# Optimization experiments

Measured on AMD Instinct MI355X. Metric: run time of the kernel, lower is better.

Reference implementation:

```python
import jax, jax.numpy as jnp
import numpy as np

N, C, H, W = 8, 256, 128, 128
K = 7            # cls_p
HID = 10         # hidden_dim
OUT_C = (K - 1) * HID  # 60
BN_EPS = 1e-5


def setup_inputs() -> dict:
    key = jax.random.key(0)
    ks = jax.random.split(key, 7)
    return {
        "p_fea": jax.random.normal(ks[0], (N, C, H, W), jnp.float32),
        "p_seg": jax.random.normal(ks[1], (N, K, H, W), jnp.float32),
        "Wq": jax.random.normal(ks[2], (HID, C), jnp.float32) * 0.05,
        "bq": jax.random.normal(ks[3], (HID,), jnp.float32) * 0.05,
        "Wk": jax.random.normal(ks[4], (HID, C), jnp.float32) * 0.05,
        "bk": jax.random.normal(ks[5], (HID,), jnp.float32) * 0.05,
        "Wp": jax.random.normal(ks[6], (OUT_C, 2 * C), jnp.float32) * 0.05,
        "gamma": jnp.ones((OUT_C,), jnp.float32),
        "beta": jnp.zeros((OUT_C,), jnp.float32),
    }


def reference(p_fea, p_seg, Wq, bq, Wk, bk, Wp, gamma, beta):
    n, c, h, w = p_fea.shape
    hw = h * w
    fea = p_fea.reshape(n, c, hw)                      # [n,c,s]
    # class-center pooling: softmax over class dim, weighted mean of features
    att = jax.nn.softmax(p_seg.reshape(n, K, hw), axis=1)      # [n,k,s]
    num = jnp.einsum('ncs,nks->nck', fea, att)                 # [n,c,k]
    den = jnp.sum(att, axis=2)[:, None, :]                     # [n,1,k]
    p_center = num / den                                        # [n,c,k]
    # 1x1 conv1d / conv2d == matmul over channel dim
    query = jnp.einsum('oc,nck->nok', Wq, p_center) + bq[None, :, None]  # [n,hid,k]
    key_ = jnp.einsum('oc,ncs->nos', Wk, fea) + bk[None, :, None]        # [n,hid,s]
    energy = jnp.einsum('nok,nos->nks', query, key_)                     # [n,k,s]
    attention = jax.nn.softmax(energy, axis=1)                           # over class dim
    new_fea = jnp.einsum('nck,nks->ncs', p_center, attention).reshape(n, c, h, w)
    # project: concat -> 1x1 conv (no bias) -> BN (batch stats) -> ReLU
    x = jnp.concatenate([p_fea, new_fea], axis=1)              # [n,2c,h,w]
    y = jnp.einsum('oc,nchw->nohw', Wp, x)                     # [n,60,h,w]
    mean = jnp.mean(y, axis=(0, 2, 3))
    var = jnp.var(y, axis=(0, 2, 3))
    y = (y - mean[None, :, None, None]) * jax.lax.rsqrt(var + BN_EPS)[None, :, None, None]
    y = y * gamma[None, :, None, None] + beta[None, :, None, None]
    y = jnp.maximum(y, 0.0)
    # torch.split(..., HID, dim=1) -> list of (cls_p-1) chunks; return as one axis
    return y.reshape(n, K - 1, HID, h, w)
```

## Files before the change

### kernel.cpp

```cpp
#include <hip/hip_runtime.h>
#include <hip/hip_bf16.h>

#define N_    8
#define C_    256
#define K_    7
#define HID_  10
#define OUTC_ 60
#define S_    16384
#define BN_EPS 1e-5f

#define OFF_PP     0
#define OFF_DP     1048576
#define OFF_EB     1052672
#define OFF_WB16   1052736
#define OFF_M2B    1151040
#define OFF_PART   1153600
#define OFF_SCL    1276480
#define OFF_SHF    1276544

#define GLDS(g, l) __builtin_amdgcn_global_load_lds( \
    (const __attribute__((address_space(1))) unsigned int*)(g), \
    (__attribute__((address_space(3))) unsigned int*)(l), 16, 0, 0)

typedef __attribute__((ext_vector_type(8))) short bfrag;
typedef __attribute__((ext_vector_type(4))) float f32x4;

static __device__ __forceinline__ unsigned short f2bf(float f) {
    __hip_bfloat16 h = __float2bfloat16(f);
    return *reinterpret_cast<unsigned short*>(&h);
}

__global__ void __launch_bounds__(256) k_pool(
        const float* __restrict__ fea, const float* __restrict__ seg,
        float* __restrict__ pp, float* __restrict__ dp) {
    int g = blockIdx.x;
    int lin = (g & 7) * 64 + (g >> 3);
    int n = lin >> 6, sl = lin & 63;
    int tid = threadIdx.x, lane = tid & 63, wv = tid >> 6;
    int r15 = lane & 15, kg = (lane >> 4) << 3, pg = (lane >> 4) << 2;
    int px0 = sl * 256;

    __shared__ unsigned short attT[16 * 256];
    __shared__ unsigned short feaB[2][256 * 32];
    __shared__ float red[4][8];

    {
        const float* sp = seg + (size_t)n * K_ * S_ + px0 + tid;
        float e[K_], mx = -1e30f;
#pragma unroll
        for (int k = 0; k < K_; k++) { e[k] = sp[(size_t)k * S_]; mx = fmaxf(mx, e[k]); }
        float sum = 0.f;
#pragma unroll
        for (int k = 0; k < K_; k++) { e[k] = __expf(e[k] - mx); sum += e[k]; }
        float inv = 1.f / sum;
#pragma unroll
        for (int k = 0; k < K_; k++) {
            e[k] *= inv;
            attT[k * 256 + tid] = f2bf(e[k]);
        }
#pragma unroll
        for (int k = 0; k < K_; k++) {
            float v = e[k];
            for (int off = 32; off; off >>= 1) v += __shfl_xor(v, off, 64);
            if (lane == 0) red[wv][k] = v;
        }
    }

    const float* fb = fea + (size_t)n * C_ * S_ + px0;
    int pq4 = (tid & 7) * 4;
    int crow = tid >> 3;

    {
        float4 s[8];
#pragma unroll
        for (int rr = 0; rr < 8; rr++)
            s[rr] = *(const float4*)(fb + (size_t)(rr * 32 + crow) * S_ + pq4);
#pragma unroll
        for (int rr = 0; rr < 8; rr++) {
            unsigned int u0 = (unsigned int)f2bf(s[rr].x) | ((unsigned int)f2bf(s[rr].y) << 16);
            unsigned int u1 = (unsigned int)f2bf(s[rr].z) | ((unsigned int)f2bf(s[rr].w) << 16);
            *(uint2*)&feaB[0][(rr * 32 + crow) * 32 + pq4] = make_uint2(u0, u1);
        }
    }
    __syncthreads();
    if (tid < K_)
        dp[(size_t)lin * 8 + tid] = red[0][tid] + red[1][tid] + red[2][tid] + red[3][tid];

    f32x4 acc[4];
#pragma unroll
    for (int mt = 0; mt < 4; mt++) acc[mt] = (f32x4)0.f;

#pragma unroll
    for (int ch = 0; ch < 8; ch++) {
        int cur = ch & 1;
        float4 s[8];
        if (ch < 7) {
#pragma unroll
            for (int rr = 0; rr < 8; rr++)
                s[rr] = *(const float4*)(fb + (size_t)(rr * 32 + crow) * S_ + (ch + 1) * 32 + pq4);
        }
        bfrag b = *(const bfrag*)&attT[r15 * 256 + ch * 32 + kg];
#pragma unroll
        for (int mt = 0; mt < 4; mt++) {
            bfrag a = *(const bfrag*)&feaB[cur][(wv * 64 + mt * 16 + r15) * 32 + kg];
            acc[mt] = __builtin_amdgcn_mfma_f32_16x16x32_bf16(a, b, acc[mt], 0, 0, 0);
        }
        if (ch < 7) {
#pragma unroll
            for (int rr = 0; rr < 8; rr++) {
                unsigned int u0 = (unsigned int)f2bf(s[rr].x) | ((unsigned int)f2bf(s[rr].y) << 16);
                unsigned int u1 = (unsigned int)f2bf(s[rr].z) | ((unsigned int)f2bf(s[rr].w) << 16);
                *(uint2*)&feaB[cur ^ 1][(rr * 32 + crow) * 32 + pq4] = make_uint2(u0, u1);
            }
        }
        __syncthreads();
    }

    if (r15 < K_) {
#pragma unroll
        for (int mt = 0; mt < 4; mt++) {
#pragma unroll
            for (int r = 0; r < 4; r++) {
                int c = wv * 64 + mt * 16 + pg + r;
                pp[((size_t)lin * 256 + c) * 8 + r15] = acc[mt][r];
            }
        }
    }
}

__global__ void k_center(const float* __restrict__ pp, const float* __restrict__ dp,
                         const float* __restrict__ Wq, const float* __restrict__ bq,
                         const float* __restrict__ Wk, const float* __restrict__ bk,
                         const float* __restrict__ Wp,
                         float* __restrict__ eb, float* __restrict__ m2b,
                         float* __restrict__ wb16) {
    int n = blockIdx.x >> 3, j = blockIdx.x & 7;
    int tid = threadIdx.x;
    __shared__ float pc[C_ * K_];
    __shared__ float ql[HID_ * K_];
    __shared__ float dinv[K_];
    if (tid < K_) {
        float d = 0.f;
        for (int s = 0; s < 64; s++) d += dp[(size_t)(n * 64 + s) * 8 + tid];
        dinv[tid] = 1.f / d;
    }
    __syncthreads();
    for (int i = tid; i < C_ * K_; i += 256) {
        int c = i / K_, k = i - c * K_;
        float v = 0.f;
        for (int s = 0; s < 64; s++)
            v += pp[((size_t)(n * 64 + s) * 256 + c) * 8 + k];
        pc[i] = v * dinv[k];
    }
    __syncthreads();
    if (tid < HID_ * K_) {
        int o = tid / K_, k = tid % K_;
        float s = bq[o];
        for (int c = 0; c < C_; c++) s += Wq[o * C_ + c] * pc[c * K_ + k];
        ql[tid] = s;
    }
    __syncthreads();
    unsigned short* wp16 = (unsigned short*)wb16 + (size_t)n * 24576;
    for (int i = j * 3072 + tid; i < (j + 1) * 3072; i += 256) {
        int ch = i / 6144, r = i - ch * 6144;
        int o = r / 72, jj = r - o * 72;
        float v = 0.f;
        if (o < 80 && jj < 64) {
            int c = ch * 64 + jj;
            if (o < 60) v = Wp[o * 2 * C_ + c];
            else if (o < 67) {
                int k = o - 60;
                for (int o2 = 0; o2 < HID_; o2++) v += ql[o2 * K_ + k] * Wk[o2 * C_ + c];
            }
        }
        wp16[i] = f2bf(v);
    }
    unsigned short* mp16 = (unsigned short*)m2b + (size_t)n * 640;
    if (tid < 80) {
        int i = j * 80 + tid;
        int o = i >> 3, k = i & 7;
        float v = 0.f;
        if (k < 7 && o < 60) {
            for (int c = 0; c < C_; c++) v += Wp[o * 2 * C_ + C_ + c] * pc[c * K_ + k];
        }
        mp16[i] = f2bf(v);
    }
    if (j == 0 && tid < K_) {
        float s = 0.f;
        for (int o = 0; o < HID_; o++) s += ql[o * K_ + tid] * bk[o];
        eb[n * K_ + tid] = s;
    }
}

__global__ void __launch_bounds__(256) k_main(
        const float* __restrict__ fea, const float* __restrict__ wb16,
        const float* __restrict__ ebias, const float* __restrict__ m2b,
        float* __restrict__ y, float* __restrict__ part) {
    int g = blockIdx.x;
    int lin = (g & 7) * 128 + (g >> 3);
    int n = lin >> 7, tile = lin & 127;
    int tid = threadIdx.x, lane = tid & 63, wv = tid >> 6;
    int r15 = lane & 15, kg = (lane >> 4) << 3, pg = (lane >> 4) << 2;

    __shared__ unsigned short wlds[2][6144];
    __shared__ unsigned short feaT[2][9216];
    __shared__ unsigned short abf[128 * 8];
    __shared__ unsigned short m2l[640];
    __shared__ float att_e[K_][128];
    __shared__ float ebl[8];
    __shared__ float redm[4][80];
    __shared__ float redq[4][80];

    const unsigned int* wsrc = (const unsigned int*)wb16 + (size_t)n * 12288;
    const unsigned int* m2s  = (const unsigned int*)m2b + (size_t)n * 320;
    for (int i = tid; i < 320; i += 256) ((unsigned int*)m2l)[i] = m2s[i];
    if (tid < K_) ebl[tid] = ebias[n * K_ + tid];

    const float* fbase = fea + (size_t)n * C_ * S_ + tile * 128;
    int cr2 = tid >> 3, h = tid & 7;

    f32x4 acc[5][2];
#pragma unroll
    for (int ot = 0; ot < 5; ot++) { acc[ot][0] = (f32x4)0.f; acc[ot][1] = (f32x4)0.f; }

#pragma unroll
    for (int rnd = 0; rnd < 3; rnd++)
        GLDS(wsrc + rnd * 1024 + wv * 256 + lane * 4,
             &((unsigned int*)wlds[0])[rnd * 1024 + wv * 256]);
    {
        const float* bp = fbase + (size_t)(cr2 * 2) * S_ + h * 16;
        float4 v0[4], v1[4];
#pragma unroll
        for (int i = 0; i < 4; i++) v0[i] = *(const float4*)(bp + i * 4);
#pragma unroll
        for (int i = 0; i < 4; i++) v1[i] = *(const float4*)(bp + S_ + i * 4);
        unsigned int* dst = (unsigned int*)feaT[0];
#pragma unroll
        for (int i = 0; i < 4; i++)
#pragma unroll
            for (int e = 0; e < 4; e++) {
                int px = h * 16 + i * 4 + e;
                dst[px * 36 + cr2] = (unsigned int)f2bf(((const float*)&v0[i])[e])
                                   | ((unsigned int)f2bf(((const float*)&v1[i])[e]) << 16);
            }
    }
    asm volatile("s_waitcnt vmcnt(0) lgkmcnt(0)" ::: "memory");
    __builtin_amdgcn_s_barrier();

#pragma unroll
    for (int ch = 0; ch < 4; ch++) {
        int bb = ch & 1;
        float4 s0[4], s1[4];
        if (ch < 3) {
#pragma unroll
            for (int rnd = 0; rnd < 3; rnd++)
                GLDS(wsrc + (ch + 1) * 3072 + rnd * 1024 + wv * 256 + lane * 4,
                     &((unsigned int*)wlds[bb ^ 1])[rnd * 1024 + wv * 256]);
            const float* bp = fbase + (size_t)((ch + 1) * 64 + cr2 * 2) * S_ + h * 16;
#pragma unroll
            for (int i = 0; i < 4; i++) s0[i] = *(const float4*)(bp + i * 4);
#pragma unroll
            for (int i = 0; i < 4; i++) s1[i] = *(const float4*)(bp + S_ + i * 4);
        }
        const unsigned short* fb = feaT[bb];
        const unsigned short* wb = wlds[bb];
#pragma unroll
        for (int ks = 0; ks < 2; ks++) {
            bfrag a0 = *(const bfrag*)&fb[(wv * 32 + r15) * 72 + ks * 32 + kg];
            bfrag a1 = *(const bfrag*)&fb[(wv * 32 + 16 + r15) * 72 + ks * 32 + kg];
#pragma unroll
            for (int ot = 0; ot < 5; ot++) {
                bfrag b = *(const bfrag*)&wb[(ot * 16 + r15) * 72 + ks * 32 + kg];
                acc[ot][0] = __builtin_amdgcn_mfma_f32_16x16x32_bf16(a0, b, acc[ot][0], 0, 0, 0);
                acc[ot][1] = __builtin_amdgcn_mfma_f32_16x16x32_bf16(a1, b, acc[ot][1], 0, 0, 0);
            }
        }
        if (ch < 3) {
            unsigned int* dst = (unsigned int*)feaT[bb ^ 1];
#pragma unroll
            for (int i = 0; i < 4; i++)
#pragma unroll
                for (int e = 0; e < 4; e++) {
                    int px = h * 16 + i * 4 + e;
                    dst[px * 36 + cr2] = (unsigned int)f2bf(((const float*)&s0[i])[e])
                                       | ((unsigned int)f2bf(((const float*)&s1[i])[e]) << 16);
                }
        }
        asm volatile("s_waitcnt vmcnt(0) lgkmcnt(0)" ::: "memory");
        __builtin_amdgcn_s_barrier();
    }

    if (r15 >= 12) {
        int k = r15 - 12;
#pragma unroll
        for (int pxt = 0; pxt < 2; pxt++)
#pragma unroll
            for (int r = 0; r < 4; r++)
                att_e[k][wv * 32 + pxt * 16 + pg + r] = acc[3][pxt][r];
    }
    if (r15 < 3) {
        int k = 4 + r15;
#pragma unroll
        for (int pxt = 0; pxt < 2; pxt++)
#pragma unroll
            for (int r = 0; r < 4; r++)
                att_e[k][wv * 32 + pxt * 16 + pg + r] = acc[4][pxt][r];
    }
    __syncthreads();
    if (tid < 128) {
        float e[K_], mx = -1e30f;
#pragma unroll
        for (int k = 0; k < K_; k++) { e[k] = att_e[k][tid] + ebl[k]; mx = fmaxf(mx, e[k]); }
        float sum = 0.f;
#pragma unroll
        for (int k = 0; k < K_; k++) { e[k] = __expf(e[k] - mx); sum += e[k]; }
        float inv = 1.f / sum;
        unsigned int* ab = (unsigned int*)abf;
        ab[tid * 4 + 0] = (unsigned int)f2bf(e[0] * inv) | ((unsigned int)f2bf(e[1] * inv) << 16);
        ab[tid * 4 + 1] = (unsigned int)f2bf(e[2] * inv) | ((unsigned int)f2bf(e[3] * inv) << 16);
        ab[tid * 4 + 2] = (unsigned int)f2bf(e[4] * inv) | ((unsigned int)f2bf(e[5] * inv) << 16);
        ab[tid * 4 + 3] = (unsigned int)f2bf(e[6] * inv);
    }
    __syncthreads();

    bfrag az = (bfrag)(short)0;
    bfrag a20 = az, a21 = az;
    if (lane < 16) {
        a20 = *(const bfrag*)&abf[(wv * 32 + r15) * 8];
        a21 = *(const bfrag*)&abf[(wv * 32 + 16 + r15) * 8];
    }
#pragma unroll
    for (int ot = 0; ot < 5; ot++) {
        bfrag b2 = az;
        if (lane < 16) b2 = *(const bfrag*)&m2l[(ot * 16 + r15) * 8];
        acc[ot][0] = __builtin_amdgcn_mfma_f32_16x16x32_bf16(a20, b2, acc[ot][0], 0, 0, 0);
        acc[ot][1] = __builtin_amdgcn_mfma_f32_16x16x32_bf16(a21, b2, acc[ot][1], 0, 0, 0);
    }

    float* ybase = y + (size_t)n * OUTC_ * S_ + tile * 128 + wv * 32 + pg;
#pragma unroll
    for (int ot = 0; ot < 5; ot++) {
        int o = ot * 16 + r15;
        float sm_ = 0.f, sq_ = 0.f;
#pragma unroll
        for (int pxt = 0; pxt < 2; pxt++) {
            f32x4 v = acc[ot][pxt];
            if (o < OUTC_)
                *(f32x4*)(ybase + (size_t)o * S_ + pxt * 16) = v;
            sm_ += v[0] + v[1] + v[2] + v[3];
            sq_ += v[0]*v[0] + v[1]*v[1] + v[2]*v[2] + v[3]*v[3];
        }
        sm_ += __shfl_xor(sm_, 16, 64); sm_ += __shfl_xor(sm_, 32, 64);
        sq_ += __shfl_xor(sq_, 16, 64); sq_ += __shfl_xor(sq_, 32, 64);
        if (lane < 16) { redm[wv][ot * 16 + lane] = sm_; redq[wv][ot * 16 + lane] = sq_; }
    }
    __syncthreads();
    if (tid < 120) {
        float s;
        if (tid < OUTC_)
            s = redm[0][tid] + redm[1][tid] + redm[2][tid] + redm[3][tid];
        else {
            int o = tid - OUTC_;
            s = redq[0][o] + redq[1][o] + redq[2][o] + redq[3][o];
        }
        part[(size_t)g * 120 + tid] = s;
    }
}

__global__ void k_bn(const float* __restrict__ part, const float* __restrict__ gamma,
                     const float* __restrict__ beta, float* __restrict__ scl,
                     float* __restrict__ shf) {
    int t = threadIdx.x & 127, q = threadIdx.x >> 7;
    __shared__ float red[4][120];
    __shared__ float tot[120];
    if (t < 120) {
        float s = 0.f;
        for (int b = q * 256; b < q * 256 + 256; b++) s += part[(size_t)b * 120 + t];
        red[q][t] = s;
    }
    __syncthreads();
    if (threadIdx.x < 120)
        tot[threadIdx.x] = red[0][threadIdx.x] + red[1][threadIdx.x] +
                           red[2][threadIdx.x] + red[3][threadIdx.x];
    __syncthreads();
    if (threadIdx.x < OUTC_) {
        const float invn = 1.f / (float)(N_ * S_);
        float mean = tot[threadIdx.x] * invn;
        float var = tot[60 + threadIdx.x] * invn - mean * mean;
        float sc = gamma[threadIdx.x] * rsqrtf(var + BN_EPS);
        scl[threadIdx.x] = sc;
        shf[threadIdx.x] = beta[threadIdx.x] - mean * sc;
    }
}

__global__ void k_apply(float* __restrict__ y, const float* __restrict__ scl,
                        const float* __restrict__ shf) {
    int idx = blockIdx.x * 256 + threadIdx.x;
    int o = (idx >> 12) % OUTC_;
    float4 v = ((const float4*)y)[idx];
    float a = scl[o], b = shf[o];
    v.x = fmaxf(v.x * a + b, 0.f);
    v.y = fmaxf(v.y * a + b, 0.f);
    v.z = fmaxf(v.z * a + b, 0.f);
    v.w = fmaxf(v.w * a + b, 0.f);
    ((float4*)y)[idx] = v;
}

extern "C" void kernel_launch(void* const* d_in, const int* in_sizes, int n_in,
                              void* d_out, int out_size, void* d_ws, size_t ws_size,
                              hipStream_t stream) {
    const float* p_fea = (const float*)d_in[0];
    const float* p_seg = (const float*)d_in[1];
    const float* Wq    = (const float*)d_in[2];
    const float* bq    = (const float*)d_in[3];
    const float* Wk    = (const float*)d_in[4];
    const float* bk    = (const float*)d_in[5];
    const float* Wp    = (const float*)d_in[6];
    const float* gamma = (const float*)d_in[7];
    const float* beta  = (const float*)d_in[8];

    float* ws   = (float*)d_ws;
    float* pp   = ws + OFF_PP;
    float* dp   = ws + OFF_DP;
    float* eb   = ws + OFF_EB;
    float* wb16 = ws + OFF_WB16;
    float* m2b  = ws + OFF_M2B;
    float* part = ws + OFF_PART;
    float* scl  = ws + OFF_SCL;
    float* shf  = ws + OFF_SHF;
    float* ybuf = (float*)d_out;

    k_pool<<<512, 256, 0, stream>>>(p_fea, p_seg, pp, dp);
    k_center<<<64, 256, 0, stream>>>(pp, dp, Wq, bq, Wk, bk, Wp, eb, m2b, wb16);
    k_main<<<1024, 256, 0, stream>>>(p_fea, wb16, eb, m2b, ybuf, part);
    k_bn<<<1, 512, 0, stream>>>(part, gamma, beta, scl, shf);
    k_apply<<<(N_ * OUTC_ * S_ / 4) / 256, 256, 0, stream>>>(ybuf, scl, shf);
}
```

Baseline: 117.7 us.

## Split pooling channels across blocks and load main-kernel weights into registers

The pooling kernel now splits the 256 channels into two halves per pixel slice, doubling the grid to 1024 blocks and halving its shared memory and accumulators. This should give better occupancy and load balance. The main kernel drops the async global-to-LDS weight staging and instead loads per-chunk weight fragments straight from global memory into registers. Its shared memory is merged into one aliased buffer to shrink the LDS footprint, which needs an extra barrier before the softmax results overwrite the aliased region. The trade-offs are recomputing the softmax over the segmentation map twice per slice and relying on cache hits for the repeated weight loads.

```diff
diff --git a/kernel.cpp b/kernel.cpp
--- a/kernel.cpp
+++ b/kernel.cpp
@@ -18,10 +18,6 @@
 #define OFF_SCL    1276480
 #define OFF_SHF    1276544
 
-#define GLDS(g, l) __builtin_amdgcn_global_load_lds( \
-    (const __attribute__((address_space(1))) unsigned int*)(g), \
-    (__attribute__((address_space(3))) unsigned int*)(l), 16, 0, 0)
-
 typedef __attribute__((ext_vector_type(8))) short bfrag;
 typedef __attribute__((ext_vector_type(4))) float f32x4;
 
@@ -34,14 +30,16 @@
         const float* __restrict__ fea, const float* __restrict__ seg,
         float* __restrict__ pp, float* __restrict__ dp) {
     int g = blockIdx.x;
-    int lin = (g & 7) * 64 + (g >> 3);
-    int n = lin >> 6, sl = lin & 63;
+    int lin = (g & 7) * 128 + (g >> 3);
+    int n = lin >> 7, r = lin & 127;
+    int sl = r >> 1, h2 = r & 1;
+    int c0 = h2 * 128;
+    int px0 = sl * 256;
     int tid = threadIdx.x, lane = tid & 63, wv = tid >> 6;
     int r15 = lane & 15, kg = (lane >> 4) << 3, pg = (lane >> 4) << 2;
-    int px0 = sl * 256;
 
     __shared__ unsigned short attT[16 * 256];
-    __shared__ unsigned short feaB[2][256 * 32];
+    __shared__ unsigned short feaB[2][128 * 32];
     __shared__ float red[4][8];
 
     {
@@ -66,48 +64,48 @@
         }
     }
 
-    const float* fb = fea + (size_t)n * C_ * S_ + px0;
+    const float* fb = fea + ((size_t)n * C_ + c0) * S_ + px0;
     int pq4 = (tid & 7) * 4;
     int crow = tid >> 3;
 
     {
-        float4 s[8];
-#pragma unroll
-        for (int rr = 0; rr < 8; rr++)
+        float4 s[4];
+#pragma unroll
+        for (int rr = 0; rr < 4; rr++)
             s[rr] = *(const float4*)(fb + (size_t)(rr * 32 + crow) * S_ + pq4);
 #pragma unroll
-        for (int rr = 0; rr < 8; rr++) {
+        for (int rr = 0; rr < 4; rr++) {
             unsigned int u0 = (unsigned int)f2bf(s[rr].x) | ((unsigned int)f2bf(s[rr].y) << 16);
             unsigned int u1 = (unsigned int)f2bf(s[rr].z) | ((unsigned int)f2bf(s[rr].w) << 16);
             *(uint2*)&feaB[0][(rr * 32 + crow) * 32 + pq4] = make_uint2(u0, u1);
         }
     }
     __syncthreads();
-    if (tid < K_)
-        dp[(size_t)lin * 8 + tid] = red[0][tid] + red[1][tid] + red[2][tid] + red[3][tid];
-
-    f32x4 acc[4];
-#pragma unroll
-    for (int mt = 0; mt < 4; mt++) acc[mt] = (f32x4)0.f;
+    if (h2 == 0 && tid < K_)
+        dp[(size_t)(n * 64 + sl) * 8 + tid] =
+            red[0][tid] + red[1][tid] + red[2][tid] + red[3][tid];
+
+    f32x4 acc[2];
+    acc[0] = (f32x4)0.f; acc[1] = (f32x4)0.f;
 
 #pragma unroll
     for (int ch = 0; ch < 8; ch++) {
         int cur = ch & 1;
-        float4 s[8];
+        float4 s[4];
         if (ch < 7) {
 #pragma unroll
-            for (int rr = 0; rr < 8; rr++)
+            for (int rr = 0; rr < 4; rr++)
                 s[rr] = *(const float4*)(fb + (size_t)(rr * 32 + crow) * S_ + (ch + 1) * 32 + pq4);
         }
         bfrag b = *(const bfrag*)&attT[r15 * 256 + ch * 32 + kg];
 #pragma unroll
-        for (int mt = 0; mt < 4; mt++) {
-            bfrag a = *(const bfrag*)&feaB[cur][(wv * 64 + mt * 16 + r15) * 32 + kg];
+        for (int mt = 0; mt < 2; mt++) {
+            bfrag a = *(const bfrag*)&feaB[cur][(wv * 32 + mt * 16 + r15) * 32 + kg];
             acc[mt] = __builtin_amdgcn_mfma_f32_16x16x32_bf16(a, b, acc[mt], 0, 0, 0);
         }
         if (ch < 7) {
 #pragma unroll
-            for (int rr = 0; rr < 8; rr++) {
+            for (int rr = 0; rr < 4; rr++) {
                 unsigned int u0 = (unsigned int)f2bf(s[rr].x) | ((unsigned int)f2bf(s[rr].y) << 16);
                 unsigned int u1 = (unsigned int)f2bf(s[rr].z) | ((unsigned int)f2bf(s[rr].w) << 16);
                 *(uint2*)&feaB[cur ^ 1][(rr * 32 + crow) * 32 + pq4] = make_uint2(u0, u1);
@@ -116,13 +114,13 @@
         __syncthreads();
     }
 
-    if (r15 < K_) {
-#pragma unroll
-        for (int mt = 0; mt < 4; mt++) {
-#pragma unroll
-            for (int r = 0; r < 4; r++) {
-                int c = wv * 64 + mt * 16 + pg + r;
-                pp[((size_t)lin * 256 + c) * 8 + r15] = acc[mt][r];
+    if (r15 < 8) {
+#pragma unroll
+        for (int mt = 0; mt < 2; mt++) {
+#pragma unroll
+            for (int rr = 0; rr < 4; rr++) {
+                int c = c0 + wv * 32 + mt * 16 + pg + rr;
+                pp[((size_t)(n * 64 + sl) * 256 + c) * 8 + r15] = acc[mt][rr];
             }
         }
     }
@@ -202,17 +200,18 @@
     int tid = threadIdx.x, lane = tid & 63, wv = tid >> 6;
     int r15 = lane & 15, kg = (lane >> 4) << 3, pg = (lane >> 4) << 2;
 
-    __shared__ unsigned short wlds[2][6144];
-    __shared__ unsigned short feaT[2][9216];
-    __shared__ unsigned short abf[128 * 8];
-    __shared__ unsigned short m2l[640];
-    __shared__ float att_e[K_][128];
-    __shared__ float ebl[8];
-    __shared__ float redm[4][80];
-    __shared__ float redq[4][80];
-
-    const unsigned int* wsrc = (const unsigned int*)wb16 + (size_t)n * 12288;
-    const unsigned int* m2s  = (const unsigned int*)m2b + (size_t)n * 320;
+    __shared__ __align__(16) unsigned char smem[38176];
+    unsigned short* feaT0 = (unsigned short*)smem;
+    unsigned short* feaT1 = (unsigned short*)(smem + 18432);
+    unsigned short* m2l   = (unsigned short*)(smem + 36864);
+    float* ebl            = (float*)(smem + 38144);
+    float* att_e          = (float*)smem;
+    unsigned short* abf   = (unsigned short*)(smem + 3584);
+    float* redm           = (float*)(smem + 5632);
+    float* redq           = (float*)(smem + 6912);
+
+    const unsigned short* wimg = (const unsigned short*)wb16 + (size_t)n * 24576;
+    const unsigned int* m2s = (const unsigned int*)m2b + (size_t)n * 320;
     for (int i = tid; i < 320; i += 256) ((unsigned int*)m2l)[i] = m2s[i];
     if (tid < K_) ebl[tid] = ebias[n * K_ + tid];
 
@@ -223,10 +222,6 @@
 #pragma unroll
     for (int ot = 0; ot < 5; ot++) { acc[ot][0] = (f32x4)0.f; acc[ot][1] = (f32x4)0.f; }
 
-#pragma unroll
-    for (int rnd = 0; rnd < 3; rnd++)
-        GLDS(wsrc + rnd * 1024 + wv * 256 + lane * 4,
-             &((unsigned int*)wlds[0])[rnd * 1024 + wv * 256]);
     {
         const float* bp = fbase + (size_t)(cr2 * 2) * S_ + h * 16;
         float4 v0[4], v1[4];
@@ -234,7 +229,7 @@
         for (int i = 0; i < 4; i++) v0[i] = *(const float4*)(bp + i * 4);
 #pragma unroll
         for (int i = 0; i < 4; i++) v1[i] = *(const float4*)(bp + S_ + i * 4);
-        unsigned int* dst = (unsigned int*)feaT[0];
+        unsigned int* dst = (unsigned int*)feaT0;
 #pragma unroll
         for (int i = 0; i < 4; i++)
 #pragma unroll
@@ -244,39 +239,39 @@
                                    | ((unsigned int)f2bf(((const float*)&v1[i])[e]) << 16);
             }
     }
-    asm volatile("s_waitcnt vmcnt(0) lgkmcnt(0)" ::: "memory");
-    __builtin_amdgcn_s_barrier();
+    __syncthreads();
 
 #pragma unroll
     for (int ch = 0; ch < 4; ch++) {
         int bb = ch & 1;
+        const unsigned short* fb = bb ? feaT1 : feaT0;
+        unsigned short* fdst = bb ? feaT0 : feaT1;
+        bfrag B[5][2];
+#pragma unroll
+        for (int ot = 0; ot < 5; ot++)
+#pragma unroll
+            for (int ks = 0; ks < 2; ks++)
+                B[ot][ks] = *(const bfrag*)&wimg[ch * 6144 + (ot * 16 + r15) * 72 + ks * 32 + kg];
         float4 s0[4], s1[4];
         if (ch < 3) {
-#pragma unroll
-            for (int rnd = 0; rnd < 3; rnd++)
-                GLDS(wsrc + (ch + 1) * 3072 + rnd * 1024 + wv * 256 + lane * 4,
-                     &((unsigned int*)wlds[bb ^ 1])[rnd * 1024 + wv * 256]);
             const float* bp = fbase + (size_t)((ch + 1) * 64 + cr2 * 2) * S_ + h * 16;
 #pragma unroll
             for (int i = 0; i < 4; i++) s0[i] = *(const float4*)(bp + i * 4);
 #pragma unroll
             for (int i = 0; i < 4; i++) s1[i] = *(const float4*)(bp + S_ + i * 4);
         }
-        const unsigned short* fb = feaT[bb];
-        const unsigned short* wb = wlds[bb];
 #pragma unroll
         for (int ks = 0; ks < 2; ks++) {
             bfrag a0 = *(const bfrag*)&fb[(wv * 32 + r15) * 72 + ks * 32 + kg];
             bfrag a1 = *(const bfrag*)&fb[(wv * 32 + 16 + r15) * 72 + ks * 32 + kg];
 #pragma unroll
             for (int ot = 0; ot < 5; ot++) {
-                bfrag b = *(const bfrag*)&wb[(ot * 16 + r15) * 72 + ks * 32 + kg];
-                acc[ot][0] = __builtin_amdgcn_mfma_f32_16x16x32_bf16(a0, b, acc[ot][0], 0, 0, 0);
-                acc[ot][1] = __builtin_amdgcn_mfma_f32_16x16x32_bf16(a1, b, acc[ot][1], 0, 0, 0);
+                acc[ot][0] = __builtin_amdgcn_mfma_f32_16x16x32_bf16(a0, B[ot][ks], acc[ot][0], 0, 0, 0);
+                acc[ot][1] = __builtin_amdgcn_mfma_f32_16x16x32_bf16(a1, B[ot][ks], acc[ot][1], 0, 0, 0);
             }
         }
         if (ch < 3) {
-            unsigned int* dst = (unsigned int*)feaT[bb ^ 1];
+            unsigned int* dst = (unsigned int*)fdst;
 #pragma unroll
             for (int i = 0; i < 4; i++)
 #pragma unroll
@@ -286,8 +281,7 @@
                                        | ((unsigned int)f2bf(((const float*)&s1[i])[e]) << 16);
                 }
         }
-        asm volatile("s_waitcnt vmcnt(0) lgkmcnt(0)" ::: "memory");
-        __builtin_amdgcn_s_barrier();
+        __syncthreads();
     }
 
     if (r15 >= 12) {
@@ -296,7 +290,7 @@
         for (int pxt = 0; pxt < 2; pxt++)
 #pragma unroll
             for (int r = 0; r < 4; r++)
-                att_e[k][wv * 32 + pxt * 16 + pg + r] = acc[3][pxt][r];
+                att_e[k * 128 + wv * 32 + pxt * 16 + pg + r] = acc[3][pxt][r];
     }
     if (r15 < 3) {
         int k = 4 + r15;
@@ -304,22 +298,27 @@
         for (int pxt = 0; pxt < 2; pxt++)
 #pragma unroll
             for (int r = 0; r < 4; r++)
-                att_e[k][wv * 32 + pxt * 16 + pg + r] = acc[4][pxt][r];
+                att_e[k * 128 + wv * 32 + pxt * 16 + pg + r] = acc[4][pxt][r];
     }
     __syncthreads();
     if (tid < 128) {
         float e[K_], mx = -1e30f;
 #pragma unroll
-        for (int k = 0; k < K_; k++) { e[k] = att_e[k][tid] + ebl[k]; mx = fmaxf(mx, e[k]); }
+        for (int k = 0; k < K_; k++) { e[k] = att_e[k * 128 + tid] + ebl[k]; mx = fmaxf(mx, e[k]); }
         float sum = 0.f;
 #pragma unroll
         for (int k = 0; k < K_; k++) { e[k] = __expf(e[k] - mx); sum += e[k]; }
         float inv = 1.f / sum;
+        unsigned int a01 = (unsigned int)f2bf(e[0] * inv) | ((unsigned int)f2bf(e[1] * inv) << 16);
+        unsigned int a23 = (unsigned int)f2bf(e[2] * inv) | ((unsigned int)f2bf(e[3] * inv) << 16);
+        unsigned int a45 = (unsigned int)f2bf(e[4] * inv) | ((unsigned int)f2bf(e[5] * inv) << 16);
+        unsigned int a6  = (unsigned int)f2bf(e[6] * inv);
+        __syncthreads();
         unsigned int* ab = (unsigned int*)abf;
-        ab[tid * 4 + 0] = (unsigned int)f2bf(e[0] * inv) | ((unsigned int)f2bf(e[1] * inv) << 16);
-        ab[tid * 4 + 1] = (unsigned int)f2bf(e[2] * inv) | ((unsigned int)f2bf(e[3] * inv) << 16);
-        ab[tid * 4 + 2] = (unsigned int)f2bf(e[4] * inv) | ((unsigned int)f2bf(e[5] * inv) << 16);
-        ab[tid * 4 + 3] = (unsigned int)f2bf(e[6] * inv);
+        ab[tid * 4 + 0] = a01; ab[tid * 4 + 1] = a23;
+        ab[tid * 4 + 2] = a45; ab[tid * 4 + 3] = a6;
+    } else {
+        __syncthreads();
     }
     __syncthreads();
 
@@ -352,16 +351,16 @@
         }
         sm_ += __shfl_xor(sm_, 16, 64); sm_ += __shfl_xor(sm_, 32, 64);
         sq_ += __shfl_xor(sq_, 16, 64); sq_ += __shfl_xor(sq_, 32, 64);
-        if (lane < 16) { redm[wv][ot * 16 + lane] = sm_; redq[wv][ot * 16 + lane] = sq_; }
+        if (lane < 16) { redm[wv * 80 + ot * 16 + lane] = sm_; redq[wv * 80 + ot * 16 + lane] = sq_; }
     }
     __syncthreads();
     if (tid < 120) {
         float s;
         if (tid < OUTC_)
-            s = redm[0][tid] + redm[1][tid] + redm[2][tid] + redm[3][tid];
+            s = redm[0 * 80 + tid] + redm[1 * 80 + tid] + redm[2 * 80 + tid] + redm[3 * 80 + tid];
         else {
             int o = tid - OUTC_;
-            s = redq[0][o] + redq[1][o] + redq[2][o] + redq[3][o];
+            s = redq[0 * 80 + o] + redq[1 * 80 + o] + redq[2 * 80 + o] + redq[3 * 80 + o];
         }
         part[(size_t)g * 120 + tid] = s;
     }
@@ -430,7 +429,7 @@
     float* shf  = ws + OFF_SHF;
     float* ybuf = (float*)d_out;
 
-    k_pool<<<512, 256, 0, stream>>>(p_fea, p_seg, pp, dp);
+    k_pool<<<1024, 256, 0, stream>>>(p_fea, p_seg, pp, dp);
     k_center<<<64, 256, 0, stream>>>(pp, dp, Wq, bq, Wk, bk, Wp, eb, m2b, wb16);
     k_main<<<1024, 256, 0, stream>>>(p_fea, wb16, eb, m2b, ybuf, part);
     k_bn<<<1, 512, 0, stream>>>(part, gamma, beta, scl, shf);
```

New measurement: 121.5 us. +3.2%, slower.
